# Optimization experiments

Measured on AMD Instinct MI355X. Metric: run time of the kernel, lower is better.

The kernel has to match this reference:

```python
import jax, jax.numpy as jnp
import numpy as np

RATE = 0.001  # matches init kwarg `rate`


def _hebbian_layer(vi, w, b, c1w, c1b, c2w, c2b, batch_num):
    # vi: (B, I), w: (O, I), b: (O,)
    vj = jax.nn.relu(vi @ w.T + b)  # (B, O) == relu(old_vj)
    # meta-MLP over the broadcasted (B, O, I) grid with 3 input channels
    # (input_stack, weight_stack, output_stack); conv1 is 1x1 so it is a
    # per-element linear map 3 -> H. We fuse the broadcast into the matmul
    # instead of materializing the stacked (B, 3, O, I) tensor.
    # c1w: (H, 3), c1b: (H,)
    h = jax.nn.relu(
        vi[:, None, :, None] * c1w[:, 0]
        + w[None, :, :, None] * c1w[:, 1]
        + vj[:, :, None, None] * c1w[:, 2]
        + c1b
    )  # (B, O, I, H)
    # conv2: H -> 1, then squeeze; scale by rate / batch_num
    shift = (h @ c2w + c2b) * (RATE / batch_num)  # (B, O, I)
    # out = old_vj + sum(input_stack * shift, dim=2)
    out = vj + jnp.sum(vi[:, None, :] * shift, axis=2)  # (B, O)
    # NOTE: torch also does layer.data += mean(shift, dim=0) as a stateful
    # side effect; it does not affect this forward pass's return value.
    return out


def setup_inputs() -> dict:
    key = jax.random.key(0)
    ks = jax.random.split(key, 9)
    B, I, Hd, O, MH = 8, 1024, 2048, 512, 8
    inp = {
        "x": jax.random.normal(ks[0], (B, I), dtype=jnp.float32),
        "w1": jax.random.normal(ks[1], (Hd, I), dtype=jnp.float32) * 0.02,
        "b1": jax.random.normal(ks[2], (Hd,), dtype=jnp.float32) * 0.02,
        "w2": jax.random.normal(ks[3], (O, Hd), dtype=jnp.float32) * 0.02,
        "b2": jax.random.normal(ks[4], (O,), dtype=jnp.float32) * 0.02,
        "c1w": jax.random.normal(ks[5], (MH, 3), dtype=jnp.float32) * 0.5,
        "c1b": jax.random.normal(ks[6], (MH,), dtype=jnp.float32) * 0.5,
        "c2w": jax.random.normal(ks[7], (MH,), dtype=jnp.float32) * 0.5,
        "c2b": jax.random.normal(ks[8], (), dtype=jnp.float32) * 0.5,
        "batch_num": 1,
    }
    return inp


def reference(x, w1, b1, w2, b2, c1w, c1b, c2w, c2b, batch_num):
    out = _hebbian_layer(x, w1, b1, c1w, c1b, c2w, c2b, batch_num)
    out = _hebbian_layer(out, w2, b2, c1w, c1b, c2w, c2b, batch_num)
    return out
```

## Files before the change

kernel.cpp:

```cpp
#include <hip/hip_runtime.h>

#define RATE 0.001f

typedef float f2 __attribute__((ext_vector_type(2)));
typedef float f4 __attribute__((ext_vector_type(4)));

static __device__ __forceinline__ f2 splat2(float v) { f2 r; r.x = v; r.y = v; return r; }
static __device__ __forceinline__ f2 vfma2(f2 a, f2 b, f2 c) { return __builtin_elementwise_fma(a, b, c); }

template<int I>
__global__ __launch_bounds__(512) void hebb_layer(
    const float* __restrict__ vi,
    const float* __restrict__ w,
    const float* __restrict__ bias,
    const float* __restrict__ c1w,
    const float* __restrict__ c1b,
    const float* __restrict__ c2w,
    const float* __restrict__ c2b_p,
    const int*   __restrict__ bn_p,
    float* __restrict__ out,
    int O)
{
    const int o    = blockIdx.x;
    const int tid  = threadIdx.x;
    const int lane = tid & 63;
    const int b    = tid >> 6;

    const float* __restrict__ wrow = w  + (size_t)o * I;
    const float* __restrict__ arow = vi + (size_t)b * I;

    constexpr int ITERS = I / 256;

    float dot = 0.f, ss = 0.f;
    for (int it = 0; it < ITERS; ++it) {
        const int base = it * 256 + lane * 4;
        const f4 wv = *(const f4*)(wrow + base);
        const f4 av = *(const f4*)(arow + base);
#pragma unroll
        for (int e = 0; e < 4; ++e) {
            dot = fmaf(av[e], wv[e], dot);
            ss += av[e];
        }
    }
#pragma unroll
    for (int off = 1; off < 64; off <<= 1) {
        dot += __shfl_xor(dot, off, 64);
        ss  += __shfl_xor(ss,  off, 64);
    }
    const float vj = fmaxf(dot + bias[o], 0.f);

    f2 p2[4], q2[4], c22[4], K2[4];
#pragma unroll
    for (int j = 0; j < 4; ++j) {
        p2[j].x  = c1w[(2*j)*3 + 0];  p2[j].y  = c1w[(2*j+1)*3 + 0];
        q2[j].x  = c1w[(2*j)*3 + 1];  q2[j].y  = c1w[(2*j+1)*3 + 1];
        c22[j].x = c2w[2*j];          c22[j].y = c2w[2*j+1];
        K2[j].x  = fmaf(vj, c1w[(2*j)*3 + 2], c1b[2*j]);
        K2[j].y  = fmaf(vj, c1w[(2*j+1)*3 + 2], c1b[2*j+1]);
    }
    const float c2b   = *c2b_p;
    const float scale = RATE / (float)(*bn_p);

    f2 acc = splat2(0.f);
    for (int it = 0; it < ITERS; ++it) {
        const int base = it * 256 + lane * 4;
        const f4 wv4 = *(const f4*)(wrow + base);
        const f4 av4 = *(const f4*)(arow + base);
#pragma unroll
        for (int e = 0; e < 4; ++e) {
            const f2 wvE = splat2(wv4[e]);
            const f2 aE  = splat2(av4[e]);
            f2 t = splat2(0.f);
#pragma unroll
            for (int j = 0; j < 4; ++j) {
                f2 z = vfma2(wvE, q2[j], K2[j]);
                z = vfma2(aE, p2[j], z);
                const f2 u = __builtin_elementwise_max(z, splat2(0.f));
                t = vfma2(u, c22[j], t);
            }
            acc = vfma2(aE, t, acc);
        }
    }
    float r = acc.x + acc.y;
#pragma unroll
    for (int off = 1; off < 64; off <<= 1) r += __shfl_xor(r, off, 64);

    if (lane == 0) out[(size_t)b * O + o] = vj + scale * (r + c2b * ss);
}

extern "C" void kernel_launch(void* const* d_in, const int* in_sizes, int n_in,
                              void* d_out, int out_size, void* d_ws, size_t ws_size,
                              hipStream_t stream) {
    const float* x   = (const float*)d_in[0];
    const float* w1  = (const float*)d_in[1];
    const float* b1  = (const float*)d_in[2];
    const float* w2  = (const float*)d_in[3];
    const float* b2  = (const float*)d_in[4];
    const float* c1w = (const float*)d_in[5];
    const float* c1b = (const float*)d_in[6];
    const float* c2w = (const float*)d_in[7];
    const float* c2b = (const float*)d_in[8];
    const int*   bn  = (const int*)d_in[9];

    float* out = (float*)d_out;
    float* mid = (float*)d_ws;

    hebb_layer<1024><<<2048, 512, 0, stream>>>(x,   w1, b1, c1w, c1b, c2w, c2b, bn, mid, 2048);
    hebb_layer<2048><<<512,  512, 0, stream>>>(mid, w2, b2, c1w, c1b, c2w, c2b, bn, out, 512);
}
```

Before: 101.1 us.

## Process two batch rows per wave with split-K halves to reuse weight loads

Each wave now handles two batch rows over half of the input dimension, so every weight vector load is reused for two rows and the loops become fully unrollable. Partial dots and accumulators are combined across the two halves through shared memory with two block barriers. The c2b term is folded into the per-element accumulator instead of a separate row-sum, and launch bounds request higher occupancy. This adds LDS traffic, barriers and register pressure from the doubled state, with the occupancy hint possibly forcing spills.

```diff
diff --git a/kernel.cpp b/kernel.cpp
--- a/kernel.cpp
+++ b/kernel.cpp
@@ -9,7 +9,7 @@
 static __device__ __forceinline__ f2 vfma2(f2 a, f2 b, f2 c) { return __builtin_elementwise_fma(a, b, c); }
 
 template<int I>
-__global__ __launch_bounds__(512) void hebb_layer(
+__global__ __launch_bounds__(512, 4) void hebb_layer(
     const float* __restrict__ vi,
     const float* __restrict__ w,
     const float* __restrict__ bias,
@@ -24,68 +24,111 @@
     const int o    = blockIdx.x;
     const int tid  = threadIdx.x;
     const int lane = tid & 63;
-    const int b    = tid >> 6;
+    const int wv8  = tid >> 6;
+    const int pr   = wv8 & 3;
+    const int half = wv8 >> 2;
 
-    const float* __restrict__ wrow = w  + (size_t)o * I;
-    const float* __restrict__ arow = vi + (size_t)b * I;
+    constexpr int HALF  = I / 2;
+    constexpr int ITERS = HALF / 256;
 
-    constexpr int ITERS = I / 256;
+    const float* __restrict__ wrow = w  + (size_t)o * I        + (size_t)half * HALF;
+    const float* __restrict__ a0   = vi + (size_t)(2*pr) * I   + (size_t)half * HALF;
+    const float* __restrict__ a1   = a0 + I;
 
-    float dot = 0.f, ss = 0.f;
+    __shared__ float dotp[8][2];
+    __shared__ float accp[8][2];
+
+    float d0 = 0.f, d1 = 0.f;
+#pragma unroll
     for (int it = 0; it < ITERS; ++it) {
         const int base = it * 256 + lane * 4;
-        const f4 wv = *(const f4*)(wrow + base);
-        const f4 av = *(const f4*)(arow + base);
+        const f4 wv4 = *(const f4*)(wrow + base);
+        const f4 a0v = *(const f4*)(a0 + base);
+        const f4 a1v = *(const f4*)(a1 + base);
 #pragma unroll
         for (int e = 0; e < 4; ++e) {
-            dot = fmaf(av[e], wv[e], dot);
-            ss += av[e];
+            d0 = fmaf(a0v[e], wv4[e], d0);
+            d1 = fmaf(a1v[e], wv4[e], d1);
         }
     }
 #pragma unroll
     for (int off = 1; off < 64; off <<= 1) {
-        dot += __shfl_xor(dot, off, 64);
-        ss  += __shfl_xor(ss,  off, 64);
+        d0 += __shfl_xor(d0, off, 64);
+        d1 += __shfl_xor(d1, off, 64);
     }
-    const float vj = fmaxf(dot + bias[o], 0.f);
+    if (lane == 0) { dotp[wv8][0] = d0; dotp[wv8][1] = d1; }
+    __syncthreads();
 
-    f2 p2[4], q2[4], c22[4], K2[4];
+    const float bo   = bias[o];
+    const float vj0  = fmaxf(dotp[pr][0] + dotp[pr + 4][0] + bo, 0.f);
+    const float vj1  = fmaxf(dotp[pr][1] + dotp[pr + 4][1] + bo, 0.f);
+    const float c2b  = *c2b_p;
+
+    f2 p2[4], q2[4], c22[4], K0[4], K1[4];
 #pragma unroll
     for (int j = 0; j < 4; ++j) {
+        const float rA = c1w[(2*j)*3 + 2], rB = c1w[(2*j+1)*3 + 2];
+        const float cA = c1b[2*j],         cB = c1b[2*j+1];
         p2[j].x  = c1w[(2*j)*3 + 0];  p2[j].y  = c1w[(2*j+1)*3 + 0];
         q2[j].x  = c1w[(2*j)*3 + 1];  q2[j].y  = c1w[(2*j+1)*3 + 1];
         c22[j].x = c2w[2*j];          c22[j].y = c2w[2*j+1];
-        K2[j].x  = fmaf(vj, c1w[(2*j)*3 + 2], c1b[2*j]);
-        K2[j].y  = fmaf(vj, c1w[(2*j+1)*3 + 2], c1b[2*j+1]);
+        K0[j].x  = fmaf(vj0, rA, cA); K0[j].y  = fmaf(vj0, rB, cB);
+        K1[j].x  = fmaf(vj1, rA, cA); K1[j].y  = fmaf(vj1, rB, cB);
     }
-    const float c2b   = *c2b_p;
-    const float scale = RATE / (float)(*bn_p);
 
-    f2 acc = splat2(0.f);
+    f2 acc0 = splat2(0.f), acc1 = splat2(0.f);
+#pragma unroll
     for (int it = 0; it < ITERS; ++it) {
         const int base = it * 256 + lane * 4;
         const f4 wv4 = *(const f4*)(wrow + base);
-        const f4 av4 = *(const f4*)(arow + base);
+        const f4 a0v = *(const f4*)(a0 + base);
+        const f4 a1v = *(const f4*)(a1 + base);
 #pragma unroll
         for (int e = 0; e < 4; ++e) {
             const f2 wvE = splat2(wv4[e]);
-            const f2 aE  = splat2(av4[e]);
-            f2 t = splat2(0.f);
+            {
+                const f2 aE = splat2(a0v[e]);
+                f2 t; t.x = c2b; t.y = 0.f;
 #pragma unroll
-            for (int j = 0; j < 4; ++j) {
-                f2 z = vfma2(wvE, q2[j], K2[j]);
-                z = vfma2(aE, p2[j], z);
-                const f2 u = __builtin_elementwise_max(z, splat2(0.f));
-                t = vfma2(u, c22[j], t);
+                for (int j = 0; j < 4; ++j) {
+                    f2 z = vfma2(wvE, q2[j], K0[j]);
+                    z = vfma2(aE, p2[j], z);
+                    const f2 u = __builtin_elementwise_max(z, splat2(0.f));
+                    t = vfma2(u, c22[j], t);
+                }
+                acc0 = vfma2(aE, t, acc0);
             }
-            acc = vfma2(aE, t, acc);
+            {
+                const f2 aE = splat2(a1v[e]);
+                f2 t; t.x = c2b; t.y = 0.f;
+#pragma unroll
+                for (int j = 0; j < 4; ++j) {
+                    f2 z = vfma2(wvE, q2[j], K1[j]);
+                    z = vfma2(aE, p2[j], z);
+                    const f2 u = __builtin_elementwise_max(z, splat2(0.f));
+                    t = vfma2(u, c22[j], t);
+                }
+                acc1 = vfma2(aE, t, acc1);
+            }
         }
     }
-    float r = acc.x + acc.y;
+    float r0 = acc0.x + acc0.y, r1 = acc1.x + acc1.y;
 #pragma unroll
-    for (int off = 1; off < 64; off <<= 1) r += __shfl_xor(r, off, 64);
+    for (int off = 1; off < 64; off <<= 1) {
+        r0 += __shfl_xor(r0, off, 64);
+        r1 += __shfl_xor(r1, off, 64);
+    }
+    if (lane == 0) { accp[wv8][0] = r0; accp[wv8][1] = r1; }
+    __syncthreads();
 
-    if (lane == 0) out[(size_t)b * O + o] = vj + scale * (r + c2b * ss);
+    if (tid < 8) {
+        const int b = tid, p = b >> 1, bb = b & 1;
+        const float dt = dotp[p][bb] + dotp[p + 4][bb];
+        const float vj = fmaxf(dt + bias[o], 0.f);
+        const float r  = accp[p][bb] + accp[p + 4][bb];
+        const float scale = RATE / (float)(*bn_p);
+        out[(size_t)b * O + o] = vj + scale * r;
+    }
 }
 
 extern "C" void kernel_launch(void* const* d_in, const int* in_sizes, int n_in,
```

Result: no change. 102.4 us (+1.3%).
